# Performance work log

Hardware: AMD Instinct MI355X
Metric: run time of the kernel (lower is better)

The kernel has to match this reference:

```python
import jax, jax.numpy as jnp
import numpy as np

DIM = 1024
NUM_HEADS = 16
HEAD_DIM = DIM // NUM_HEADS
SCALE = HEAD_DIM ** -0.5


def setup_inputs() -> dict:
    key = jax.random.key(0)
    ks = jax.random.split(key, 7)
    b, n = 2, 2048
    x = jax.random.normal(ks[0], (b, n, DIM), dtype=jnp.float32)
    s = DIM ** -0.5
    Wq = jax.random.normal(ks[1], (DIM, DIM), dtype=jnp.float32) * s
    bq = jax.random.normal(ks[2], (DIM,), dtype=jnp.float32) * 0.01
    Wk = jax.random.normal(ks[3], (DIM, DIM), dtype=jnp.float32) * s
    bk = jax.random.normal(ks[4], (DIM,), dtype=jnp.float32) * 0.01
    Wv = jax.random.normal(ks[5], (DIM, DIM), dtype=jnp.float32) * s
    bv = jax.random.normal(ks[6], (DIM,), dtype=jnp.float32) * 0.01
    return {"x": x, "Wq": Wq, "bq": bq, "Wk": Wk, "bk": bk, "Wv": Wv, "bv": bv}


def reference(x, Wq, bq, Wk, bk, Wv, bv):
    b, n, _ = x.shape
    # Linear projections (torch Linear: x @ W.T + b; here W stored as [in, out])
    q = x @ Wq + bq
    k = x @ Wk + bk
    v = x @ Wv + bv
    # split heads: [b, n, h*d] -> [b, h, n, d]
    split = lambda t: t.reshape(b, n, NUM_HEADS, HEAD_DIM).transpose(0, 2, 1, 3)
    q, k, v = split(q), split(k), split(v)
    sim = jnp.einsum('bhid,bhjd->bhij', q, k) * SCALE
    attn = jax.nn.softmax(sim, axis=-1)
    out = jnp.einsum('bhij,bhjd->bhid', attn, v)
    return out.transpose(0, 2, 1, 3).reshape(b, n, DIM)
```

## Files before the change

kernel.cpp:

```cpp
#include <hip/hip_runtime.h>
#include <cstdint>
#include <cstddef>

#define NB    2
#define SEQ   2048
#define DIMC  1024
#define NH    16
#define HDIM  64
#define MROWS (NB*SEQ)
#define NFEAT (3*DIMC)
#define KVBLK 64
#define NT    (SEQ/KVBLK)

typedef _Float16 half8 __attribute__((ext_vector_type(8)));
typedef _Float16 half4 __attribute__((ext_vector_type(4)));
typedef _Float16 half2v __attribute__((ext_vector_type(2)));
typedef __fp16   fp16x2 __attribute__((ext_vector_type(2)));
typedef float    f32x4 __attribute__((ext_vector_type(4)));

typedef const __attribute__((address_space(1))) void* gas_ptr;
typedef __attribute__((address_space(3))) void*       las_ptr;

__device__ __forceinline__ void gload_lds16(const void* g, void* l) {
    __builtin_amdgcn_global_load_lds((gas_ptr)g, (las_ptr)l, 16, 0, 0);
}

__device__ __forceinline__ int swz4(int r) { return (r ^ (r >> 2)) & 3; }

__device__ __forceinline__ float fast_exp2(float x) {
    float r;
    asm("v_exp_f32 %0, %1" : "=v"(r) : "v"(x));
    return r;
}

__device__ __forceinline__ half2v pk_f16(float a, float b) {
    fp16x2 r = __builtin_amdgcn_cvt_pkrtz(a, b);
    return __builtin_bit_cast(half2v, r);
}

__global__ __launch_bounds__(256) void k_convert_x(const float* __restrict__ x,
                                                   _Float16* __restrict__ x16) {
    int i = (blockIdx.x * 256 + threadIdx.x) * 4;
    float4 v = *reinterpret_cast<const float4*>(x + i);
    half4 h = { (_Float16)v.x, (_Float16)v.y, (_Float16)v.z, (_Float16)v.w };
    *reinterpret_cast<half4*>(x16 + i) = h;
}

__global__ __launch_bounds__(256) void k_transpose_w(const float* __restrict__ Wq,
                                                     const float* __restrict__ Wk,
                                                     const float* __restrict__ Wv,
                                                     _Float16* __restrict__ wt) {
    __shared__ float tile[64][65];
    const int bid  = blockIdx.x;
    const int midx = bid >> 8;
    const int t2   = bid & 255;
    const int i0   = (t2 >> 4) * 64;
    const int o0   = (t2 & 15) * 64;
    const float* W = (midx == 0) ? Wq : (midx == 1 ? Wk : Wv);
    const int tid  = threadIdx.x;
    #pragma unroll
    for (int p = 0; p < 4; ++p) {
        int id = p * 256 + tid;
        int r = id >> 4, c4 = (id & 15) * 4;
        float4 v = *reinterpret_cast<const float4*>(W + (size_t)(i0 + r) * DIMC + o0 + c4);
        tile[r][c4 + 0] = v.x; tile[r][c4 + 1] = v.y;
        tile[r][c4 + 2] = v.z; tile[r][c4 + 3] = v.w;
    }
    __syncthreads();
    #pragma unroll
    for (int p = 0; p < 4; ++p) {
        int id = p * 256 + tid;
        int oc = id >> 4, i4 = (id & 15) * 4;
        half4 h = { (_Float16)tile[i4 + 0][oc], (_Float16)tile[i4 + 1][oc],
                    (_Float16)tile[i4 + 2][oc], (_Float16)tile[i4 + 3][oc] };
        *reinterpret_cast<half4*>(wt + (size_t)(midx * DIMC + o0 + oc) * DIMC + i0 + i4) = h;
    }
}

__global__ __launch_bounds__(256) void k_qkv_gemm(
    const _Float16* __restrict__ x16, const _Float16* __restrict__ wt,
    const float* __restrict__ bq, const float* __restrict__ bk, const float* __restrict__ bv,
    _Float16* __restrict__ q16, _Float16* __restrict__ k16, _Float16* __restrict__ vt16)
{
    __shared__ __align__(16) char sraw[34816];
    const int tid = threadIdx.x;
    const int lane = tid & 63;
    const int w = tid >> 6, wm = w >> 1, wn = w & 1;
    const int lr = lane & 15, lg = lane >> 4;
    const int bn = blockIdx.x % (NFEAT / 128);
    const int bm = blockIdx.x / (NFEAT / 128);
    const int m0 = bm * 128, n0 = bn * 128;

    const f32x4 zero4 = {0.f, 0.f, 0.f, 0.f};
    f32x4 acc[4][4];
    #pragma unroll
    for (int i = 0; i < 4; ++i)
        #pragma unroll
        for (int j = 0; j < 4; ++j) acc[i][j] = zero4;

    auto stage = [&](int buf, int kt) {
        const int k0 = kt * 32;
        char* Adst = sraw + buf * 8192;
        char* Bdst = sraw + 16384 + buf * 8192;
        #pragma unroll
        for (int t = 0; t < 2; ++t) {
            int slot = t * 256 + tid;
            int row = slot >> 2, ch = slot & 3;
            int chg = ch ^ swz4(row);
            gload_lds16(x16 + (size_t)(m0 + row) * DIMC + k0 + chg * 8, Adst + slot * 16);
            gload_lds16(wt  + (size_t)(n0 + row) * DIMC + k0 + chg * 8, Bdst + slot * 16);
        }
    };

    stage(0, 0);
    for (int kt = 0; kt < DIMC / 32; ++kt) {
        __syncthreads();
        if (kt + 1 < DIMC / 32) stage((kt + 1) & 1, kt + 1);
        const char* Ab = sraw + (kt & 1) * 8192;
        const char* Bb = sraw + 16384 + (kt & 1) * 8192;
        half8 af[4], bf[4];
        #pragma unroll
        for (int mb = 0; mb < 4; ++mb) {
            int row = wm * 64 + mb * 16 + lr;
            af[mb] = *(const half8*)(Ab + row * 64 + ((lg ^ swz4(row)) << 4));
        }
        #pragma unroll
        for (int nb = 0; nb < 4; ++nb) {
            int col = wn * 64 + nb * 16 + lr;
            bf[nb] = *(const half8*)(Bb + col * 64 + ((lg ^ swz4(col)) << 4));
        }
        #pragma unroll
        for (int mb = 0; mb < 4; ++mb)
            #pragma unroll
            for (int nb = 0; nb < 4; ++nb)
                acc[mb][nb] = __builtin_amdgcn_mfma_f32_16x16x32_f16(af[mb], bf[nb], acc[mb][nb], 0, 0, 0);
    }

    const int sec = n0 >> 10;
    const float* bias = (sec == 0) ? bq : (sec == 1 ? bk : bv);
    const float scl = (sec == 0) ? 0.125f * 1.44269504088896f : 1.0f;
    float bfv[4];
    #pragma unroll
    for (int nb = 0; nb < 4; ++nb)
        bfv[nb] = bias[(n0 & 1023) + wn * 64 + nb * 16 + lr];

    if (sec < 2) {
        _Float16* dst = (sec == 0) ? q16 : k16;
        #pragma unroll
        for (int mb = 0; mb < 4; ++mb)
            #pragma unroll
            for (int i2 = 0; i2 < 4; ++i2) {
                int rg = m0 + wm * 64 + mb * 16 + lg * 4 + i2;
                int bb = rg >> 11, nn = rg & (SEQ - 1);
                #pragma unroll
                for (int nb = 0; nb < 4; ++nb) {
                    int f1 = (n0 & 1023) + wn * 64 + nb * 16 + lr;
                    int hh = f1 >> 6, dd = f1 & 63;
                    dst[((size_t)(bb * NH + hh) * SEQ + nn) * HDIM + dd] =
                        (_Float16)((acc[mb][nb][i2] + bfv[nb]) * scl);
                }
            }
    } else {
        __syncthreads();
        char* lt = sraw;
        #pragma unroll
        for (int mb = 0; mb < 4; ++mb)
            #pragma unroll
            for (int nb = 0; nb < 4; ++nb) {
                int c  = wn * 64 + nb * 16 + lr;
                int r0 = wm * 64 + mb * 16 + lg * 4;
                half4 hv = { (_Float16)(acc[mb][nb][0] + bfv[nb]),
                             (_Float16)(acc[mb][nb][1] + bfv[nb]),
                             (_Float16)(acc[mb][nb][2] + bfv[nb]),
                             (_Float16)(acc[mb][nb][3] + bfv[nb]) };
                *(half4*)(lt + c * 272 + r0 * 2) = hv;
            }
        __syncthreads();
        #pragma unroll
        for (int p = 0; p < 8; ++p) {
            int id = p * 256 + tid;
            int c = id >> 4, r8 = (id & 15) * 8;
            half8 hv = *(const half8*)(lt + c * 272 + r8 * 2);
            int f1 = (n0 & 1023) + c;
            int hh = f1 >> 6, dd = f1 & 63;
            int rg = m0 + r8;
            int bb = rg >> 11, nn = rg & (SEQ - 1);
            *(half8*)(vt16 + ((size_t)(bb * NH + hh) * HDIM + dd) * SEQ + nn) = hv;
        }
    }
}

__global__ __launch_bounds__(512) void k_attn(
    const _Float16* __restrict__ q16, const _Float16* __restrict__ k16,
    const _Float16* __restrict__ vt16, float* __restrict__ out)
{
    __shared__ __align__(16) char lds[49152];
    const int tid = threadIdx.x, lane = tid & 63, w = tid >> 6;
    const int lr = lane & 15, lg = lane >> 4;
    const int bh = blockIdx.x >> 4;
    const int qt = blockIdx.x & 15;
    const int qrow0 = qt * 128 + w * 16;
    const _Float16* qh = q16 + (size_t)bh * SEQ * HDIM;
    const _Float16* kh = k16 + (size_t)bh * SEQ * HDIM;
    const _Float16* vh = vt16 + (size_t)bh * HDIM * SEQ;
    char* pl = lds + 32768 + w * 2048;

    const int srow = tid >> 3;
    const int scg  = (tid & 7) ^ (srow & 7);

    auto stageKV = [&](int buf, int j0) {
        gload_lds16(kh + (size_t)(j0 + srow) * HDIM + scg * 8,
                    lds + buf * 8192 + tid * 16);
        gload_lds16(vh + (size_t)srow * SEQ + j0 + scg * 8,
                    lds + 16384 + buf * 8192 + tid * 16);
    };

    half8 aq[2];
    #pragma unroll
    for (int kc = 0; kc < 2; ++kc)
        aq[kc] = *(const half8*)(qh + (size_t)(qrow0 + lr) * HDIM + kc * 32 + lg * 8);

    const f32x4 zero4 = {0.f, 0.f, 0.f, 0.f};
    float m_i = -1e30f, l_i = 0.f;
    f32x4 oacc[4];
    #pragma unroll
    for (int i = 0; i < 4; ++i) oacc[i] = zero4;

    stageKV(0, 0);
    for (int t = 0; t < NT; ++t) {
        const int j0 = t * KVBLK;
        __syncthreads();
        if (t + 1 < NT) stageKV((t + 1) & 1, j0 + KVBLK);
        const char* Kb = lds + (t & 1) * 8192;
        const char* Vb = lds + 16384 + (t & 1) * 8192;

        f32x4 s[4];
        __builtin_amdgcn_s_setprio(1);
        #pragma unroll
        for (int jb = 0; jb < 4; ++jb) {
            int row = jb * 16 + lr;
            half8 k0 = *(const half8*)(Kb + row * 128 + (((0 + lg) ^ (row & 7)) << 4));
            half8 k1 = *(const half8*)(Kb + row * 128 + (((4 + lg) ^ (row & 7)) << 4));
            f32x4 sa = zero4;
            sa = __builtin_amdgcn_mfma_f32_16x16x32_f16(k0, aq[0], sa, 0, 0, 0);
            sa = __builtin_amdgcn_mfma_f32_16x16x32_f16(k1, aq[1], sa, 0, 0, 0);
            s[jb] = sa;
        }
        __builtin_amdgcn_s_setprio(0);

        half8 vf[4][2];
        #pragma unroll
        for (int db = 0; db < 4; ++db)
            #pragma unroll
            for (int kc = 0; kc < 2; ++kc) {
                int row = db * 16 + lr;
                vf[db][kc] = *(const half8*)(Vb + row * 128 + (((kc * 4 + lg) ^ (row & 7)) << 4));
            }

        f32x4 mx = s[0];
        #pragma unroll
        for (int jb = 1; jb < 4; ++jb) {
            mx[0] = fmaxf(mx[0], s[jb][0]); mx[1] = fmaxf(mx[1], s[jb][1]);
            mx[2] = fmaxf(mx[2], s[jb][2]); mx[3] = fmaxf(mx[3], s[jb][3]);
        }
        float pmax = fmaxf(fmaxf(mx[0], mx[1]), fmaxf(mx[2], mx[3]));
        pmax = fmaxf(pmax, __shfl_xor(pmax, 16));
        pmax = fmaxf(pmax, __shfl_xor(pmax, 32));

        if (!__all(pmax - m_i <= 8.0f)) {
            float mn = fmaxf(m_i, pmax);
            float fac = fast_exp2(m_i - mn);
            m_i = mn;
            l_i *= fac;
            float f0 = __shfl(fac, lg * 4 + 0);
            float f1 = __shfl(fac, lg * 4 + 1);
            float f2 = __shfl(fac, lg * 4 + 2);
            float f3 = __shfl(fac, lg * 4 + 3);
            #pragma unroll
            for (int db = 0; db < 4; ++db) {
                oacc[db][0] *= f0; oacc[db][1] *= f1;
                oacc[db][2] *= f2; oacc[db][3] *= f3;
            }
        }

        #pragma unroll
        for (int jb = 0; jb < 4; ++jb)
            #pragma unroll
            for (int i = 0; i < 4; ++i)
                s[jb][i] = fast_exp2(s[jb][i] - m_i);
        f32x4 sv = s[0] + s[1] + s[2] + s[3];
        float psum = (sv[0] + sv[1]) + (sv[2] + sv[3]);
        psum += __shfl_xor(psum, 16);
        psum += __shfl_xor(psum, 32);
        l_i += psum;

        #pragma unroll
        for (int jb = 0; jb < 4; ++jb) {
            half2v w0 = pk_f16(s[jb][0], s[jb][1]);
            half2v w1 = pk_f16(s[jb][2], s[jb][3]);
            half4 pk = { w0.x, w0.y, w1.x, w1.y };
            *(half4*)(pl + lr * 128 + (((jb * 2 + (lg >> 1)) ^ (lr & 7)) << 4) + ((lg & 1) << 3)) = pk;
        }
        asm volatile("s_waitcnt lgkmcnt(0)" ::: "memory");
        half8 ap0 = *(const half8*)(pl + lr * 128 + (((0 + lg) ^ (lr & 7)) << 4));
        half8 ap1 = *(const half8*)(pl + lr * 128 + (((4 + lg) ^ (lr & 7)) << 4));
        __builtin_amdgcn_s_setprio(1);
        #pragma unroll
        for (int db = 0; db < 4; ++db) {
            oacc[db] = __builtin_amdgcn_mfma_f32_16x16x32_f16(ap0, vf[db][0], oacc[db], 0, 0, 0);
            oacc[db] = __builtin_amdgcn_mfma_f32_16x16x32_f16(ap1, vf[db][1], oacc[db], 0, 0, 0);
        }
        __builtin_amdgcn_s_setprio(0);
    }

    const int bb = bh >> 4, hh = bh & 15;
    float rlq[4];
    #pragma unroll
    for (int i = 0; i < 4; ++i)
        rlq[i] = 1.0f / __shfl(l_i, lg * 4 + i);
    #pragma unroll
    for (int db = 0; db < 4; ++db)
        #pragma unroll
        for (int i = 0; i < 4; ++i) {
            int nn = qrow0 + lg * 4 + i;
            out[((size_t)bb * SEQ + nn) * DIMC + hh * HDIM + db * 16 + lr] = oacc[db][i] * rlq[i];
        }
}

extern "C" void kernel_launch(void* const* d_in, const int* in_sizes, int n_in,
                              void* d_out, int out_size, void* d_ws, size_t ws_size,
                              hipStream_t stream)
{
    const float* x  = (const float*)d_in[0];
    const float* Wq = (const float*)d_in[1];
    const float* bq = (const float*)d_in[2];
    const float* Wk = (const float*)d_in[3];
    const float* bk = (const float*)d_in[4];
    const float* Wv = (const float*)d_in[5];
    const float* bv = (const float*)d_in[6];
    float* out = (float*)d_out;

    char* ws = (char*)d_ws;
    _Float16* x16  = (_Float16*)ws;
    _Float16* wt   = (_Float16*)(ws + ((size_t)8  << 20));
    _Float16* q16  = (_Float16*)(ws + ((size_t)14 << 20));
    _Float16* k16  = (_Float16*)(ws + ((size_t)22 << 20));
    _Float16* vt16 = (_Float16*)(ws + ((size_t)30 << 20));

    k_convert_x<<<MROWS * DIMC / 1024, 256, 0, stream>>>(x, x16);
    k_transpose_w<<<3 * 256, 256, 0, stream>>>(Wq, Wk, Wv, wt);
    k_qkv_gemm<<<(MROWS / 128) * (NFEAT / 128), 256, 0, stream>>>(x16, wt, bq, bk, bv,
                                                                  q16, k16, vt16);
    k_attn<<<32 * (SEQ / 128), 512, 0, stream>>>(q16, k16, vt16, out);
}
```

Before: 102.0 us.

## Halve attention query tile to 64 rows, swizzle blocks, fix P LDS bank conflicts

The attention kernel now uses 4-wave blocks that each own 64 query rows instead of 8-wave blocks with 128 rows, so it launches twice as many blocks. Each thread stages two K/V chunks per tile, which costs more redundant K/V traffic per query row. Block indices are remapped so consecutive blocks spread across heads, likely to balance load across XCDs and caches. The P-tile LDS writes and reads get an extra half-swizzle to reduce bank conflicts, at the price of four half4 reads in place of two half8 reads.

```diff
diff --git a/kernel.cpp b/kernel.cpp
--- a/kernel.cpp
+++ b/kernel.cpp
@@ -190,29 +190,34 @@
     }
 }
 
-__global__ __launch_bounds__(512) void k_attn(
+__global__ __launch_bounds__(256) void k_attn(
     const _Float16* __restrict__ q16, const _Float16* __restrict__ k16,
     const _Float16* __restrict__ vt16, float* __restrict__ out)
 {
-    __shared__ __align__(16) char lds[49152];
+    __shared__ __align__(16) char lds[40960];
     const int tid = threadIdx.x, lane = tid & 63, w = tid >> 6;
     const int lr = lane & 15, lg = lane >> 4;
-    const int bh = blockIdx.x >> 4;
-    const int qt = blockIdx.x & 15;
-    const int qrow0 = qt * 128 + w * 16;
+    const int swz = (blockIdx.x & 7) * 128 + (blockIdx.x >> 3);
+    const int bh = swz >> 5;
+    const int qt = swz & 31;
+    const int qrow0 = qt * 64 + w * 16;
     const _Float16* qh = q16 + (size_t)bh * SEQ * HDIM;
     const _Float16* kh = k16 + (size_t)bh * SEQ * HDIM;
     const _Float16* vh = vt16 + (size_t)bh * HDIM * SEQ;
     char* pl = lds + 32768 + w * 2048;
-
-    const int srow = tid >> 3;
-    const int scg  = (tid & 7) ^ (srow & 7);
+    const int rb = lr >> 3;
 
     auto stageKV = [&](int buf, int j0) {
-        gload_lds16(kh + (size_t)(j0 + srow) * HDIM + scg * 8,
-                    lds + buf * 8192 + tid * 16);
-        gload_lds16(vh + (size_t)srow * SEQ + j0 + scg * 8,
-                    lds + 16384 + buf * 8192 + tid * 16);
+        #pragma unroll
+        for (int t = 0; t < 2; ++t) {
+            int slot = t * 256 + tid;
+            int row  = slot >> 3;
+            int chg  = (slot & 7) ^ (row & 7);
+            gload_lds16(kh + (size_t)(j0 + row) * HDIM + chg * 8,
+                        lds + buf * 8192 + slot * 16);
+            gload_lds16(vh + (size_t)row * SEQ + j0 + chg * 8,
+                        lds + 16384 + buf * 8192 + slot * 16);
+        }
     };
 
     half8 aq[2];
@@ -299,11 +304,17 @@
             half2v w0 = pk_f16(s[jb][0], s[jb][1]);
             half2v w1 = pk_f16(s[jb][2], s[jb][3]);
             half4 pk = { w0.x, w0.y, w1.x, w1.y };
-            *(half4*)(pl + lr * 128 + (((jb * 2 + (lg >> 1)) ^ (lr & 7)) << 4) + ((lg & 1) << 3)) = pk;
+            *(half4*)(pl + lr * 128 + (((jb * 2 + (lg >> 1)) ^ (lr & 7)) << 4)
+                      + (((lg & 1) ^ rb) << 3)) = pk;
         }
         asm volatile("s_waitcnt lgkmcnt(0)" ::: "memory");
-        half8 ap0 = *(const half8*)(pl + lr * 128 + (((0 + lg) ^ (lr & 7)) << 4));
-        half8 ap1 = *(const half8*)(pl + lr * 128 + (((4 + lg) ^ (lr & 7)) << 4));
+        const char* prow = pl + lr * 128;
+        half4 l0 = *(const half4*)(prow + (((0 + lg) ^ (lr & 7)) << 4) + (rb << 3));
+        half4 h0 = *(const half4*)(prow + (((0 + lg) ^ (lr & 7)) << 4) + ((1 ^ rb) << 3));
+        half4 l1 = *(const half4*)(prow + (((4 + lg) ^ (lr & 7)) << 4) + (rb << 3));
+        half4 h1 = *(const half4*)(prow + (((4 + lg) ^ (lr & 7)) << 4) + ((1 ^ rb) << 3));
+        half8 ap0 = { l0.x, l0.y, l0.z, l0.w, h0.x, h0.y, h0.z, h0.w };
+        half8 ap1 = { l1.x, l1.y, l1.z, l1.w, h1.x, h1.y, h1.z, h1.w };
         __builtin_amdgcn_s_setprio(1);
         #pragma unroll
         for (int db = 0; db < 4; ++db) {
@@ -351,5 +362,5 @@
     k_transpose_w<<<3 * 256, 256, 0, stream>>>(Wq, Wk, Wv, wt);
     k_qkv_gemm<<<(MROWS / 128) * (NFEAT / 128), 256, 0, stream>>>(x16, wt, bq, bk, bv,
                                                                   q16, k16, vt16);
-    k_attn<<<32 * (SEQ / 128), 512, 0, stream>>>(q16, k16, vt16, out);
-}
+    k_attn<<<32 * (SEQ / 64), 256, 0, stream>>>(q16, k16, vt16, out);
+}
```

New measurement: 121.2 us. 1.19x slower.
